# Kernel tuning notes

Hardware: AMD Instinct MI355X
Metric: run time of the kernel (lower is better)

## Reference

```python
import jax, jax.numpy as jnp
import numpy as np

N_EMBD = 384
N_HEAD = 6
HEAD_SIZE = N_EMBD // N_HEAD
D_FF = 4 * N_EMBD
LN_EPS = 1e-3  # keras LayerNormalization default epsilon


def setup_inputs() -> dict:
    key = jax.random.key(0)
    ks = jax.random.split(key, 12)
    B, T = 4, 2048
    s = 1.0 / np.sqrt(N_EMBD)
    return {
        "x": jax.random.normal(ks[0], (B, T, N_EMBD), dtype=jnp.float32),
        "Wq": jax.random.normal(ks[1], (N_EMBD, N_EMBD), dtype=jnp.float32) * s,
        "Wk": jax.random.normal(ks[2], (N_EMBD, N_EMBD), dtype=jnp.float32) * s,
        "Wv": jax.random.normal(ks[3], (N_EMBD, N_EMBD), dtype=jnp.float32) * s,
        "Wo": jax.random.normal(ks[4], (N_EMBD, N_EMBD), dtype=jnp.float32) * s,
        "bo": jnp.zeros((N_EMBD,), dtype=jnp.float32),
        "W1": jax.random.normal(ks[5], (N_EMBD, D_FF), dtype=jnp.float32) * s,
        "b1": jnp.zeros((D_FF,), dtype=jnp.float32),
        "W2": jax.random.normal(ks[6], (D_FF, N_EMBD), dtype=jnp.float32) * (1.0 / np.sqrt(D_FF)),
        "b2": jnp.zeros((N_EMBD,), dtype=jnp.float32),
        "g1": jnp.ones((N_EMBD,), dtype=jnp.float32),
        "be1": jnp.zeros((N_EMBD,), dtype=jnp.float32),
        "g2": jnp.ones((N_EMBD,), dtype=jnp.float32),
        "be2": jnp.zeros((N_EMBD,), dtype=jnp.float32),
    }


def _layer_norm(x, gamma, beta):
    mu = jnp.mean(x, axis=-1, keepdims=True)
    var = jnp.mean(jnp.square(x - mu), axis=-1, keepdims=True)
    return (x - mu) * jax.lax.rsqrt(var + LN_EPS) * gamma + beta


def _block(x, Wq, Wk, Wv, Wo, bo, W1, b1, W2, b2, g1, be1, g2, be2):
    B, T, C = x.shape
    H, D = N_HEAD, HEAD_SIZE
    q = (x @ Wq).reshape(B, T, H, D).transpose(0, 2, 1, 3)  # [B,H,T,D]
    k = (x @ Wk).reshape(B, T, H, D).transpose(0, 2, 1, 3)
    v = (x @ Wv).reshape(B, T, H, D).transpose(0, 2, 1, 3)
    scores = jnp.einsum("bhqd,bhkd->bhqk", q, k) / jnp.sqrt(jnp.float32(D))
    causal = jnp.tril(jnp.ones((T, T), dtype=bool))
    scores = jnp.where(causal, scores, jnp.float32(-1e9))
    attn = jax.nn.softmax(scores, axis=-1)  # dropout is identity at inference
    out = jnp.einsum("bhqk,bhkd->bhqd", attn, v)
    out = out.transpose(0, 2, 1, 3).reshape(B, T, H * D)
    y = out @ Wo + bo
    x = _layer_norm(x + y, g1, be1)
    y = jax.nn.relu(x @ W1 + b1) @ W2 + b2
    return _layer_norm(x + y, g2, be2)


def reference(x, Wq, Wk, Wv, Wo, bo, W1, b1, W2, b2, g1, be1, g2, be2):
    return _block(x, Wq, Wk, Wv, Wo, bo, W1, b1, W2, b2, g1, be1, g2, be2)
```

## Files before the change

### kernel.cpp

```cpp
#include <hip/hip_runtime.h>

#define C_DIM  384
#define HEADS  6
#define HD     64
#define FF_DIM 1536
#define LN_EPS 1e-3f
#define TSEQ   2048
#define BATCH  4
#define LOG2E  1.4426950408889634f
#define QK_SCALE 0.18033688011112042f

typedef __attribute__((ext_vector_type(2))) float          f32x2;
typedef __attribute__((ext_vector_type(4))) float          f32x4;
typedef __attribute__((ext_vector_type(4))) float          float4_t;
typedef __attribute__((ext_vector_type(8))) short          bfrag;
typedef __attribute__((ext_vector_type(4))) unsigned short ushort4_t;
typedef __attribute__((ext_vector_type(8))) unsigned short ushort8_t;

__device__ inline unsigned short f2bf(float f) {
    unsigned int u = __builtin_bit_cast(unsigned int, f);
    u += 0x7fff + ((u >> 16) & 1);
    return (unsigned short)(u >> 16);
}
__device__ inline unsigned short f2bf_t(float f) {
    return (unsigned short)(__builtin_bit_cast(unsigned int, f) >> 16);
}
__device__ inline float bf2f(unsigned short u) {
    return __builtin_bit_cast(float, (unsigned int)u << 16);
}

__device__ inline void gload_lds16(const void* g, void* l) {
    __builtin_amdgcn_global_load_lds(
        (const __attribute__((address_space(1))) unsigned int*)g,
        (__attribute__((address_space(3))) unsigned int*)l,
        16, 0, 0);
}

__device__ inline int xcd_chunk(int flat, int nwg) {
    return (flat >> 3) + (flat & 7) * (nwg >> 3);
}

__global__ __launch_bounds__(256)
void prep_all(const float* __restrict__ Wq, const float* __restrict__ Wk,
              const float* __restrict__ Wv, const float* __restrict__ Wo,
              const float* __restrict__ W1, const float* __restrict__ W2,
              const float* __restrict__ x,
              unsigned short* __restrict__ Dqkv, unsigned short* __restrict__ Do_,
              unsigned short* __restrict__ D1, unsigned short* __restrict__ D2,
              unsigned short* __restrict__ xb)
{
    __shared__ float tile[32][33];
    const int bidx = blockIdx.x;
    const int tx = threadIdx.x, ty = threadIdx.y;
    if (bidx >= 1728) {
        const int i = (bidx - 1728) * 256 + ty * 32 + tx;
        float4_t v = ((const float4_t*)x)[i];
        ushort4_t o = { f2bf(v.x), f2bf(v.y), f2bf(v.z), f2bf(v.w) };
        ((ushort4_t*)xb)[i] = o;
        return;
    }
    const float* W; unsigned short* D;
    int K, N, nx, ny;
    if (bidx < 576) {
        const int z = bidx / 144, r = bidx % 144;
        W = z == 0 ? Wq : (z == 1 ? Wk : (z == 2 ? Wv : Wo));
        D = z == 3 ? Do_ : Dqkv + (size_t)z * C_DIM * C_DIM;
        K = N = C_DIM; nx = r % 12; ny = r / 12;
    } else if (bidx < 1152) {
        const int r = bidx - 576;
        W = W1; D = D1; K = C_DIM; N = FF_DIM; nx = r % 48; ny = r / 48;
    } else {
        const int r = bidx - 1152;
        W = W2; D = D2; K = FF_DIM; N = C_DIM; nx = r % 12; ny = r / 12;
    }
    const int n0 = nx * 32, k0 = ny * 32;
    #pragma unroll
    for (int i = 0; i < 32; i += 8)
        tile[ty + i][tx] = W[(size_t)(k0 + ty + i) * N + n0 + tx];
    __syncthreads();
    #pragma unroll
    for (int i = 0; i < 32; i += 8)
        D[(size_t)(n0 + ty + i) * K + k0 + tx] = f2bf(tile[tx][ty + i]);
}

__global__ __launch_bounds__(256)
void vtrans_kernel(const unsigned short* __restrict__ qkv,
                   unsigned short* __restrict__ vt)
{
    __shared__ unsigned short tile[32][34];
    const int tx = threadIdx.x, ty = threadIdx.y;
    const int bh = blockIdx.z, b = bh / HEADS, h = bh % HEADS;
    const int t0 = blockIdx.x * 32, d0 = blockIdx.y * 32;
    #pragma unroll
    for (int i = 0; i < 32; i += 8)
        tile[ty + i][tx] = qkv[(size_t)(b * TSEQ + t0 + ty + i) * 1152 + 2 * C_DIM + h * HD + d0 + tx];
    __syncthreads();
    #pragma unroll
    for (int i = 0; i < 32; i += 8)
        vt[((size_t)bh * HD + d0 + ty + i) * TSEQ + t0 + tx] = tile[tx][ty + i];
}

template<int OBF16, int BIAS, int RELU, int QSCALE, int KSPLIT>
__global__ __launch_bounds__(256)
void gemm_lds(const unsigned short* __restrict__ A, const unsigned short* __restrict__ Bt,
              const float* __restrict__ bias, void* __restrict__ Cv,
              unsigned short* __restrict__ ktc,
              int M, int N, int K)
{
    __shared__ __align__(16) unsigned short As[16 * 512];
    __shared__ __align__(16) unsigned short Bs[16 * 512];

    const int t = threadIdx.x, lane = t & 63, w = t >> 6;
    const int ln16 = lane & 15, hi16 = lane >> 4;
    const int wr = w >> 1, wc = w & 1;
    const int nwg = gridDim.x * gridDim.y;
    const int L = xcd_chunk(blockIdx.y * gridDim.x + blockIdx.x, nwg);
    const int row0 = (L / gridDim.x) * 128, col0 = (L % gridDim.x) * 128;

    f32x4 acc[4][4] = {};

    for (int k0 = 0; k0 < K; k0 += 64) {
        #pragma unroll
        for (int i = 0; i < 4; ++i) {
            const int f  = w * 4 + i;
            const int ks = f >> 3, rf = f & 7;
            const int row = rf * 16 + ln16;
            const int kc  = k0 + ks * 32 + hi16 * 8;
            gload_lds16(&A [(size_t)(row0 + row) * K + kc], &As[f * 512]);
            gload_lds16(&Bt[(size_t)(col0 + row) * K + kc], &Bs[f * 512]);
        }
        __syncthreads();
        #pragma unroll
        for (int ks = 0; ks < 2; ++ks) {
            bfrag a[4], b[4];
            #pragma unroll
            for (int i = 0; i < 4; ++i)
                a[i] = *(const bfrag*)&As[(ks * 8 + wr * 4 + i) * 512 + lane * 8];
            #pragma unroll
            for (int j = 0; j < 4; ++j)
                b[j] = *(const bfrag*)&Bs[(ks * 8 + wc * 4 + j) * 512 + lane * 8];
            #pragma unroll
            for (int i = 0; i < 4; ++i)
                #pragma unroll
                for (int j = 0; j < 4; ++j)
                    acc[i][j] = __builtin_amdgcn_mfma_f32_16x16x32_bf16(a[i], b[j], acc[i][j], 0, 0, 0);
        }
        __syncthreads();
    }

    #pragma unroll
    for (int j = 0; j < 4; ++j) {
        const int cbase = col0 + wc * 64 + j * 16;
        const int col = cbase + ln16;
        const float bv = BIAS ? bias[col] : 0.0f;
        const float sc = (QSCALE && col < C_DIM) ? QK_SCALE : 1.0f;
        const bool kdest = KSPLIT && (cbase >= C_DIM) && (cbase < 2 * C_DIM);
        #pragma unroll
        for (int i = 0; i < 4; ++i) {
            #pragma unroll
            for (int e = 0; e < 4; ++e) {
                const int row = row0 + wr * 64 + i * 16 + hi16 * 4 + e;
                float v = acc[i][j][e] + bv;
                if (RELU) v = fmaxf(v, 0.0f);
                if (QSCALE) v *= sc;
                if (kdest) {
                    const int b  = row >> 11, tt = row & 2047;
                    const int hd = col - C_DIM;
                    const int bh = b * HEADS + (hd >> 6);
                    ktc[((size_t)bh * TSEQ + tt) * HD + (hd & 63)] = f2bf(v);
                } else if (OBF16) {
                    ((unsigned short*)Cv)[(size_t)row * N + col] = f2bf(v);
                } else {
                    ((float*)Cv)[(size_t)row * N + col] = v;
                }
            }
        }
    }
}

template<int OBF16, int BIAS, int RELU>
__global__ __launch_bounds__(256)
void gemm_lds64(const unsigned short* __restrict__ A, const unsigned short* __restrict__ Bt,
                const float* __restrict__ bias, void* __restrict__ Cv,
                int M, int N, int K)
{
    __shared__ __align__(16) unsigned short As[2][8 * 512];
    __shared__ __align__(16) unsigned short Bs[2][16 * 512];

    const int t = threadIdx.x, lane = t & 63, w = t >> 6;
    const int ln16 = lane & 15, hi16 = lane >> 4;
    const int wr = w >> 1, wc = w & 1;
    const int nwg = gridDim.x * gridDim.y;
    const int L = xcd_chunk(blockIdx.y * gridDim.x + blockIdx.x, nwg);
    const int row0 = (L / gridDim.x) * 64, col0 = (L % gridDim.x) * 128;

    f32x4 acc[2][4] = {};

    auto stage = [&](int bf, int k0) {
        #pragma unroll
        for (int i = 0; i < 2; ++i) {
            const int f  = w * 2 + i;
            const int ks = f >> 2, rf = f & 3;
            gload_lds16(&A[(size_t)(row0 + rf * 16 + ln16) * K + k0 + ks * 32 + hi16 * 8],
                        &As[bf][f * 512]);
        }
        #pragma unroll
        for (int i = 0; i < 4; ++i) {
            const int f  = w * 4 + i;
            const int ks = f >> 3, cf = f & 7;
            gload_lds16(&Bt[(size_t)(col0 + cf * 16 + ln16) * K + k0 + ks * 32 + hi16 * 8],
                        &Bs[bf][f * 512]);
        }
    };

    int buf = 0;
    stage(0, 0);
    __syncthreads();

    for (int k0 = 0; k0 < K; k0 += 64) {
        if (k0 + 64 < K) stage(buf ^ 1, k0 + 64);
        #pragma unroll
        for (int ks = 0; ks < 2; ++ks) {
            bfrag a[2], b[4];
            #pragma unroll
            for (int i = 0; i < 2; ++i)
                a[i] = *(const bfrag*)&As[buf][(ks * 4 + wr * 2 + i) * 512 + lane * 8];
            #pragma unroll
            for (int j = 0; j < 4; ++j)
                b[j] = *(const bfrag*)&Bs[buf][(ks * 8 + wc * 4 + j) * 512 + lane * 8];
            #pragma unroll
            for (int i = 0; i < 2; ++i)
                #pragma unroll
                for (int j = 0; j < 4; ++j)
                    acc[i][j] = __builtin_amdgcn_mfma_f32_16x16x32_bf16(a[i], b[j], acc[i][j], 0, 0, 0);
        }
        __syncthreads();
        buf ^= 1;
    }

    #pragma unroll
    for (int j = 0; j < 4; ++j) {
        const int col = col0 + wc * 64 + j * 16 + ln16;
        const float bv = BIAS ? bias[col] : 0.0f;
        #pragma unroll
        for (int i = 0; i < 2; ++i) {
            #pragma unroll
            for (int e = 0; e < 4; ++e) {
                const int row = row0 + wr * 32 + i * 16 + hi16 * 4 + e;
                float v = acc[i][j][e] + bv;
                if (RELU) v = fmaxf(v, 0.0f);
                if (OBF16) ((unsigned short*)Cv)[(size_t)row * N + col] = f2bf(v);
                else       ((float*)Cv)[(size_t)row * N + col] = v;
            }
        }
    }
}

__device__ inline void qk16(const bfrag (&qf)[2][2], const bfrag (&kf)[4][2],
                            f32x4 (&sf)[2][4])
{
    __builtin_amdgcn_s_setprio(1);
    #pragma unroll
    for (int jt = 0; jt < 4; ++jt)
        #pragma unroll
        for (int ks = 0; ks < 2; ++ks) {
            sf[0][jt] = __builtin_amdgcn_mfma_f32_16x16x32_bf16(qf[0][ks], kf[jt][ks], sf[0][jt], 0, 0, 0);
            sf[1][jt] = __builtin_amdgcn_mfma_f32_16x16x32_bf16(qf[1][ks], kf[jt][ks], sf[1][jt], 0, 0, 0);
        }
    __builtin_amdgcn_s_setprio(0);
}

__device__ inline void softmax_pv(f32x4 (&sf)[2][4], const bfrag (&vf)[4][2],
                                  f32x4 (&acc)[2][4],
                                  float (&mrow)[2][4], float (&lrow)[2][4],
                                  unsigned short (*Ps)[72],
                                  int tok0, int kt, bool last, int ln16, int hi16)
{
    float lmax[2][4];
    bool need = false;
    #pragma unroll
    for (int rf = 0; rf < 2; ++rf)
        #pragma unroll
        for (int e = 0; e < 4; ++e) {
            const int row = tok0 + rf * 16 + hi16 * 4 + e;
            float mx = -1e30f;
            #pragma unroll
            for (int jt = 0; jt < 4; ++jt) {
                float sv = sf[rf][jt][e];
                if (last && (kt * 64 + jt * 16 + ln16 > row)) sv = -1e30f;
                mx = fmaxf(mx, sv);
            }
            lmax[rf][e] = mx;
            need = need || (mx > mrow[rf][e] + 8.0f);
        }
    if (__any(need)) {
        #pragma unroll
        for (int rf = 0; rf < 2; ++rf)
            #pragma unroll
            for (int e = 0; e < 4; ++e) {
                float rm = lmax[rf][e];
                rm = fmaxf(rm, __shfl_xor(rm, 1));
                rm = fmaxf(rm, __shfl_xor(rm, 2));
                rm = fmaxf(rm, __shfl_xor(rm, 4));
                rm = fmaxf(rm, __shfl_xor(rm, 8));
                const float mn = fmaxf(mrow[rf][e], rm);
                const float corr = exp2f(mrow[rf][e] - mn);
                mrow[rf][e] = mn;
                lrow[rf][e] *= corr;
                #pragma unroll
                for (int dt = 0; dt < 4; ++dt) acc[rf][dt][e] *= corr;
            }
    }

    #pragma unroll
    for (int rf = 0; rf < 2; ++rf)
        #pragma unroll
        for (int jt = 0; jt < 4; ++jt)
            #pragma unroll
            for (int e = 0; e < 4; ++e) {
                const int row = tok0 + rf * 16 + hi16 * 4 + e;
                float sv = sf[rf][jt][e];
                if (last && (kt * 64 + jt * 16 + ln16 > row)) sv = -1e30f;
                const float pe = exp2f(sv - mrow[rf][e]);
                lrow[rf][e] += pe;
                Ps[rf * 16 + hi16 * 4 + e][jt * 16 + ln16] = f2bf_t(pe);
            }

    bfrag pf[2][2];
    #pragma unroll
    for (int rf = 0; rf < 2; ++rf)
        #pragma unroll
        for (int ks = 0; ks < 2; ++ks)
            pf[rf][ks] = *(const bfrag*)&Ps[rf * 16 + ln16][ks * 32 + hi16 * 8];
    __builtin_amdgcn_s_setprio(1);
    #pragma unroll
    for (int ks = 0; ks < 2; ++ks)
        #pragma unroll
        for (int rf = 0; rf < 2; ++rf)
            #pragma unroll
            for (int dt = 0; dt < 4; ++dt)
                acc[rf][dt] = __builtin_amdgcn_mfma_f32_16x16x32_bf16(pf[rf][ks], vf[dt][ks], acc[rf][dt], 0, 0, 0);
    __builtin_amdgcn_s_setprio(0);
}

__global__ __launch_bounds__(64)
void attn_kernel(const unsigned short* __restrict__ qkv,
                 const unsigned short* __restrict__ ktc,
                 const unsigned short* __restrict__ vt,
                 unsigned short* __restrict__ att,
                 unsigned short* __restrict__ pacc,
                 float* __restrict__ pml)
{
    __shared__ __align__(16) unsigned short Ps[32][72];
    const int lane = threadIdx.x;
    const int ln16 = lane & 15, hi16 = lane >> 4;
    const int bid = blockIdx.x;
    const int xcd = bid & 7;
    const int i   = bid >> 3;
    int bh, qw, kt0, kte, ck = 0;
    bool heavy;
    if (i < 192) {
        qw = 63 - (i / 6);
        const int r = i % 6;
        bh = xcd * 3 + (r >> 1);
        ck = r & 1;
        const int NT = (qw >> 1) + 1;
        const int half = NT >> 1;
        kt0 = ck ? half : 0;
        kte = ck ? NT : half;
        heavy = true;
    } else {
        const int j = i - 192;
        qw = 31 - (j / 3);
        bh = xcd * 3 + (j % 3);
        kt0 = 0;
        kte = (qw >> 1) + 1;
        heavy = false;
    }
    const int NTfull = (qw >> 1) + 1;
    const int b = bh / HEADS, h = bh % HEADS;
    const int tok0 = qw * 32;
    const size_t qrow0 = (size_t)b * TSEQ;

    bfrag qf[2][2];
    #pragma unroll
    for (int rf = 0; rf < 2; ++rf)
        #pragma unroll
        for (int ks = 0; ks < 2; ++ks)
            qf[rf][ks] = *(const bfrag*)&qkv[(qrow0 + tok0 + rf * 16 + ln16) * 1152 + h * HD + ks * 32 + hi16 * 8];

    f32x4 acc[2][4] = {};
    float mrow[2][4], lrow[2][4];
    #pragma unroll
    for (int rf = 0; rf < 2; ++rf)
        #pragma unroll
        for (int e = 0; e < 4; ++e) { mrow[rf][e] = -1e30f; lrow[rf][e] = 0.0f; }

    const unsigned short* Kb = ktc + (size_t)bh * TSEQ * HD;
    const unsigned short* Vb = vt  + (size_t)bh * HD * TSEQ;

    bfrag kf[4][2];
    #pragma unroll
    for (int jt = 0; jt < 4; ++jt)
        #pragma unroll
        for (int ks = 0; ks < 2; ++ks)
            kf[jt][ks] = *(const bfrag*)&Kb[(size_t)(kt0 * 64 + jt * 16 + ln16) * HD + ks * 32 + hi16 * 8];

    for (int kt = kt0; kt < kte; ++kt) {
        bfrag vf[4][2];
        #pragma unroll
        for (int dt = 0; dt < 4; ++dt)
            #pragma unroll
            for (int ks = 0; ks < 2; ++ks)
                vf[dt][ks] = *(const bfrag*)&Vb[(size_t)(dt * 16 + ln16) * TSEQ + kt * 64 + ks * 32 + hi16 * 8];

        f32x4 sf[2][4] = {};
        qk16(qf, kf, sf);

        if (kt + 1 < kte) {
            #pragma unroll
            for (int jt = 0; jt < 4; ++jt)
                #pragma unroll
                for (int ks = 0; ks < 2; ++ks)
                    kf[jt][ks] = *(const bfrag*)&Kb[(size_t)((kt + 1) * 64 + jt * 16 + ln16) * HD + ks * 32 + hi16 * 8];
        }

        softmax_pv(sf, vf, acc, mrow, lrow, Ps, tok0, kt, kt == NTfull - 1, ln16, hi16);
    }

    float lsum[2][4];
    #pragma unroll
    for (int rf = 0; rf < 2; ++rf)
        #pragma unroll
        for (int e = 0; e < 4; ++e) {
            float l = lrow[rf][e];
            l += __shfl_xor(l, 1);
            l += __shfl_xor(l, 2);
            l += __shfl_xor(l, 4);
            l += __shfl_xor(l, 8);
            lsum[rf][e] = l;
        }

    if (!heavy) {
        #pragma unroll
        for (int rf = 0; rf < 2; ++rf)
            #pragma unroll
            for (int e = 0; e < 4; ++e) {
                const float inv = 1.0f / lsum[rf][e];
                const size_t row = qrow0 + tok0 + rf * 16 + hi16 * 4 + e;
                #pragma unroll
                for (int dt = 0; dt < 4; ++dt)
                    att[row * C_DIM + h * HD + dt * 16 + ln16] = f2bf(acc[rf][dt][e] * inv);
            }
    } else {
        const int sidx = bh * 32 + (qw - 32);
        const size_t pb = (size_t)sidx * 2 + ck;
        #pragma unroll
        for (int rf = 0; rf < 2; ++rf)
            #pragma unroll
            for (int dt = 0; dt < 4; ++dt)
                #pragma unroll
                for (int e = 0; e < 4; ++e) {
                    const int row = rf * 16 + hi16 * 4 + e;
                    pacc[(pb * 32 + row) * 64 + dt * 16 + ln16] = f2bf(acc[rf][dt][e]);
                }
        if (ln16 == 0) {
            #pragma unroll
            for (int rf = 0; rf < 2; ++rf)
                #pragma unroll
                for (int e = 0; e < 4; ++e) {
                    const int row = rf * 16 + hi16 * 4 + e;
                    pml[pb * 64 + row * 2 + 0] = mrow[rf][e];
                    pml[pb * 64 + row * 2 + 1] = lsum[rf][e];
                }
        }
    }
}

__global__ __launch_bounds__(256)
void attn_combine(const unsigned short* __restrict__ pacc,
                  const float* __restrict__ pml,
                  unsigned short* __restrict__ att)
{
    const int sidx = blockIdx.x;
    const int bh = sidx >> 5;
    const int qw = 32 + (sidx & 31);
    const int b = bh / HEADS, h = bh % HEADS;
    const int tid = threadIdx.x;
    const int row = tid >> 3;
    const int d0  = (tid & 7) * 8;

    const float m0 = pml[((size_t)sidx * 2 + 0) * 64 + row * 2 + 0];
    const float l0 = pml[((size_t)sidx * 2 + 0) * 64 + row * 2 + 1];
    const float m1 = pml[((size_t)sidx * 2 + 1) * 64 + row * 2 + 0];
    const float l1 = pml[((size_t)sidx * 2 + 1) * 64 + row * 2 + 1];
    const float M  = fmaxf(m0, m1);
    const float w0 = exp2f(m0 - M), w1 = exp2f(m1 - M);
    const float invL = 1.0f / (l0 * w0 + l1 * w1);

    ushort8_t a0 = *(const ushort8_t*)&pacc[(((size_t)sidx * 2 + 0) * 32 + row) * 64 + d0];
    ushort8_t a1 = *(const ushort8_t*)&pacc[(((size_t)sidx * 2 + 1) * 32 + row) * 64 + d0];
    ushort8_t rv;
    #pragma unroll
    for (int k = 0; k < 8; ++k) {
        const float v0 = bf2f(a0[k]);
        const float v1 = bf2f(a1[k]);
        rv[k] = f2bf((v0 * w0 + v1 * w1) * invL);
    }
    const size_t grow = (size_t)b * TSEQ + qw * 32 + row;
    *(ushort8_t*)&att[grow * C_DIM + h * HD + d0] = rv;
}

template<int ABF16, int WF32, int WBF>
__global__ __launch_bounds__(256)
void ln_residual_kernel(const void* __restrict__ Av, const float* __restrict__ R,
                        const float* __restrict__ gamma, const float* __restrict__ beta,
                        float* __restrict__ out, unsigned short* __restrict__ outb, int Mrows)
{
    const int lane = threadIdx.x & 63;
    const int wv   = threadIdx.x >> 6;
    const int row  = blockIdx.x * 4 + wv;
    if (row >= Mrows) return;
    const size_t off = (size_t)row * C_DIM;

    float v[6];
    float sum = 0.0f;
    #pragma unroll
    for (int j = 0; j < 3; ++j) {
        const int c = lane * 2 + 128 * j;
        float a0, a1;
        if (ABF16) {
            const unsigned int u = *(const unsigned int*)&((const unsigned short*)Av)[off + c];
            a0 = bf2f((unsigned short)(u & 0xffff));
            a1 = bf2f((unsigned short)(u >> 16));
        } else {
            f32x2 a = *(const f32x2*)&((const float*)Av)[off + c];
            a0 = a.x; a1 = a.y;
        }
        f32x2 r = *(const f32x2*)&R[off + c];
        v[2 * j]     = a0 + r.x;
        v[2 * j + 1] = a1 + r.y;
        sum += v[2 * j] + v[2 * j + 1];
    }
    #pragma unroll
    for (int o = 1; o < 64; o <<= 1) sum += __shfl_xor(sum, o);
    const float mu = sum * (1.0f / C_DIM);

    float sq = 0.0f;
    #pragma unroll
    for (int j = 0; j < 6; ++j) { const float d = v[j] - mu; sq = fmaf(d, d, sq); }
    #pragma unroll
    for (int o = 1; o < 64; o <<= 1) sq += __shfl_xor(sq, o);
    const float rstd = rsqrtf(sq * (1.0f / C_DIM) + LN_EPS);

    #pragma unroll
    for (int j = 0; j < 3; ++j) {
        const int c = lane * 2 + 128 * j;
        f32x2 g  = *(const f32x2*)&gamma[c];
        f32x2 be = *(const f32x2*)&beta[c];
        const float r0 = (v[2 * j]     - mu) * rstd * g.x + be.x;
        const float r1 = (v[2 * j + 1] - mu) * rstd * g.y + be.y;
        if (WF32) { f32x2 o = { r0, r1 }; *(f32x2*)&out[off + c] = o; }
        if (WBF) {
            const unsigned int o = (unsigned int)f2bf(r0) | ((unsigned int)f2bf(r1) << 16);
            *(unsigned int*)&outb[off + c] = o;
        }
    }
}

extern "C" void kernel_launch(void* const* d_in, const int* in_sizes, int n_in,
                              void* d_out, int out_size, void* d_ws, size_t ws_size,
                              hipStream_t stream)
{
    const float* x   = (const float*)d_in[0];
    const float* Wq  = (const float*)d_in[1];
    const float* Wk  = (const float*)d_in[2];
    const float* Wv  = (const float*)d_in[3];
    const float* Wo  = (const float*)d_in[4];
    const float* bo  = (const float*)d_in[5];
    const float* W1  = (const float*)d_in[6];
    const float* b1  = (const float*)d_in[7];
    const float* W2  = (const float*)d_in[8];
    const float* b2  = (const float*)d_in[9];
    const float* g1  = (const float*)d_in[10];
    const float* be1 = (const float*)d_in[11];
    const float* g2  = (const float*)d_in[12];
    const float* be2 = (const float*)d_in[13];
    float* out = (float*)d_out;

    const int M = BATCH * TSEQ;
    const size_t MC = (size_t)M * C_DIM;

    char* ws = (char*)d_ws;
    unsigned short* qkv = (unsigned short*)ws;
    unsigned short* vt  = (unsigned short*)(ws + (size_t)M*1152*2);
    unsigned short* att = (unsigned short*)(ws + (size_t)M*1152*2 + (size_t)BATCH*HEADS*HD*TSEQ*2);
    unsigned short* h1  = (unsigned short*)ws;
    char* p2 = ws + (size_t)M*1152*2 + (size_t)BATCH*HEADS*HD*TSEQ*2 + MC*2;
    unsigned short* xb  = (unsigned short*)p2;
    float* y   = (float*)(p2 + MC*2);
    unsigned short* ktc = (unsigned short*)(p2 + MC*2 + MC*4);
    unsigned short* x1b = (unsigned short*)(p2 + MC*2 + 2*MC*4);
    char* p3 = p2 + MC*2 + 2*MC*4 + MC*2;
    unsigned short* Wqkv_t = (unsigned short*)p3;
    unsigned short* Wo_t   = Wqkv_t + (size_t)3*C_DIM*C_DIM;
    unsigned short* W1_t   = Wo_t   + (size_t)C_DIM*C_DIM;
    unsigned short* W2_t   = W1_t   + (size_t)FF_DIM*C_DIM;

    unsigned short* pacc = (unsigned short*)(p2 + MC*2);
    float* pml = (float*)(p2 + MC*2 + (size_t)1536*32*64*2);

    dim3 b256(256), b328(32, 8);

    prep_all<<<dim3(1728 + 3072), b328, 0, stream>>>(
        Wq, Wk, Wv, Wo, W1, W2, x, Wqkv_t, Wo_t, W1_t, W2_t, xb);

    gemm_lds<1, 0, 0, 1, 1><<<dim3(3*C_DIM/128, M/128), b256, 0, stream>>>(
        xb, Wqkv_t, nullptr, qkv, ktc, M, 3*C_DIM, C_DIM);

    vtrans_kernel<<<dim3(TSEQ/32, HD/32, BATCH*HEADS), b328, 0, stream>>>(qkv, vt);

    attn_kernel<<<dim3(2304), dim3(64), 0, stream>>>(qkv, ktc, vt, att, pacc, pml);
    attn_combine<<<dim3(768), b256, 0, stream>>>(pacc, pml, att);

    gemm_lds64<0, 1, 0><<<dim3(C_DIM/128, M/64), b256, 0, stream>>>(
        att, Wo_t, bo, y, M, C_DIM, C_DIM);

    ln_residual_kernel<0, 0, 1><<<dim3(M/4), b256, 0, stream>>>(
        x, y, g1, be1, nullptr, x1b, M);

    gemm_lds<1, 1, 1, 0, 0><<<dim3(FF_DIM/128, M/128), b256, 0, stream>>>(
        x1b, W1_t, b1, h1, nullptr, M, FF_DIM, C_DIM);

    gemm_lds64<0, 1, 0><<<dim3(C_DIM/128, M/64), b256, 0, stream>>>(
        h1, W2_t, b2, y, M, C_DIM, FF_DIM);

    ln_residual_kernel<1, 1, 0><<<dim3(M/4), b256, 0, stream>>>(
        x1b, y, g2, be2, out, nullptr, M);
}
```

Measured before the change: 191.9 us.

## Share K/V tiles across eight waves in LDS and drop split-K attention combine

Replaces the single-wave attention kernel with 512-thread blocks where eight waves each own a 32-row query slice of a 256-row tile, sharing double-buffered swizzled K/V tiles loaded to LDS via direct global-to-LDS loads. This removes redundant global K/V reads per wave and eliminates the split-KV partial write plus the separate combine kernel. The cost is only 192 blocks, fewer than the previous 2304, and causal imbalance inside a block: early-row waves sit idle at barriers while later waves finish their longer key ranges. The grid is also small relative to the CU count, so load balance across the device may suffer.

```diff
diff --git a/kernel.cpp b/kernel.cpp
--- a/kernel.cpp
+++ b/kernel.cpp
@@ -343,43 +343,29 @@
     __builtin_amdgcn_s_setprio(0);
 }
 
-__global__ __launch_bounds__(64)
-void attn_kernel(const unsigned short* __restrict__ qkv,
-                 const unsigned short* __restrict__ ktc,
-                 const unsigned short* __restrict__ vt,
-                 unsigned short* __restrict__ att,
-                 unsigned short* __restrict__ pacc,
-                 float* __restrict__ pml)
-{
-    __shared__ __align__(16) unsigned short Ps[32][72];
-    const int lane = threadIdx.x;
+__global__ __launch_bounds__(512)
+void attn8_kernel(const unsigned short* __restrict__ qkv,
+                  const unsigned short* __restrict__ ktc,
+                  const unsigned short* __restrict__ vt,
+                  unsigned short* __restrict__ att)
+{
+    __shared__ __align__(16) unsigned short Klds[2][4096];
+    __shared__ __align__(16) unsigned short Vlds[2][4096];
+    __shared__ __align__(16) unsigned short Ps[8][32][72];
+
+    const int tid  = threadIdx.x;
+    const int lane = tid & 63, wid = tid >> 6;
     const int ln16 = lane & 15, hi16 = lane >> 4;
     const int bid = blockIdx.x;
     const int xcd = bid & 7;
     const int i   = bid >> 3;
-    int bh, qw, kt0, kte, ck = 0;
-    bool heavy;
-    if (i < 192) {
-        qw = 63 - (i / 6);
-        const int r = i % 6;
-        bh = xcd * 3 + (r >> 1);
-        ck = r & 1;
-        const int NT = (qw >> 1) + 1;
-        const int half = NT >> 1;
-        kt0 = ck ? half : 0;
-        kte = ck ? NT : half;
-        heavy = true;
-    } else {
-        const int j = i - 192;
-        qw = 31 - (j / 3);
-        bh = xcd * 3 + (j % 3);
-        kt0 = 0;
-        kte = (qw >> 1) + 1;
-        heavy = false;
-    }
-    const int NTfull = (qw >> 1) + 1;
+    const int bh  = xcd * 3 + (i % 3);
+    const int qt  = 7 - (i / 3);
+    const int s   = qt * 8 + wid;
+    const int tok0 = s * 32;
+    const int NTw   = (s >> 1) + 1;
+    const int NTmax = qt * 4 + 4;
     const int b = bh / HEADS, h = bh % HEADS;
-    const int tok0 = qw * 32;
     const size_t qrow0 = (size_t)b * TSEQ;
 
     bfrag qf[2][2];
@@ -399,36 +385,50 @@
     const unsigned short* Kb = ktc + (size_t)bh * TSEQ * HD;
     const unsigned short* Vb = vt  + (size_t)bh * HD * TSEQ;
 
-    bfrag kf[4][2];
+    int off[4][2];
     #pragma unroll
     for (int jt = 0; jt < 4; ++jt)
         #pragma unroll
-        for (int ks = 0; ks < 2; ++ks)
-            kf[jt][ks] = *(const bfrag*)&Kb[(size_t)(kt0 * 64 + jt * 16 + ln16) * HD + ks * 32 + hi16 * 8];
-
-    for (int kt = kt0; kt < kte; ++kt) {
-        bfrag vf[4][2];
-        #pragma unroll
-        for (int dt = 0; dt < 4; ++dt)
-            #pragma unroll
-            for (int ks = 0; ks < 2; ++ks)
-                vf[dt][ks] = *(const bfrag*)&Vb[(size_t)(dt * 16 + ln16) * TSEQ + kt * 64 + ks * 32 + hi16 * 8];
-
-        f32x4 sf[2][4] = {};
-        qk16(qf, kf, sf);
-
-        if (kt + 1 < kte) {
+        for (int ks = 0; ks < 2; ++ks) {
+            const int row = jt * 16 + ln16;
+            off[jt][ks] = row * 128 + ((ks * 64 + hi16 * 16) ^ ((row & 7) << 4));
+        }
+
+    auto stage = [&](int bf, int kt) {
+        const int r   = tid >> 3;
+        const int s16 = (tid & 7) ^ (r & 7);
+        gload_lds16(&Kb[(size_t)(kt * 64 + r) * HD + s16 * 8], &Klds[bf][wid * 512]);
+        gload_lds16(&Vb[(size_t)r * TSEQ + kt * 64 + s16 * 8], &Vlds[bf][wid * 512]);
+    };
+
+    int buf = 0;
+    stage(0, 0);
+    __syncthreads();
+
+    for (int kt = 0; kt < NTmax; ++kt) {
+        if (kt + 1 < NTmax) stage(buf ^ 1, kt + 1);
+
+        if (kt < NTw) {
+            const char* Kb8 = (const char*)&Klds[buf][0];
+            const char* Vb8 = (const char*)&Vlds[buf][0];
+            bfrag kf[4][2], vf[4][2];
             #pragma unroll
             for (int jt = 0; jt < 4; ++jt)
                 #pragma unroll
-                for (int ks = 0; ks < 2; ++ks)
-                    kf[jt][ks] = *(const bfrag*)&Kb[(size_t)((kt + 1) * 64 + jt * 16 + ln16) * HD + ks * 32 + hi16 * 8];
-        }
-
-        softmax_pv(sf, vf, acc, mrow, lrow, Ps, tok0, kt, kt == NTfull - 1, ln16, hi16);
-    }
-
-    float lsum[2][4];
+                for (int ks = 0; ks < 2; ++ks) {
+                    kf[jt][ks] = *(const bfrag*)(Kb8 + off[jt][ks]);
+                    vf[jt][ks] = *(const bfrag*)(Vb8 + off[jt][ks]);
+                }
+
+            f32x4 sf[2][4] = {};
+            qk16(qf, kf, sf);
+            softmax_pv(sf, vf, acc, mrow, lrow, Ps[wid], tok0, kt, kt == NTw - 1, ln16, hi16);
+        }
+
+        __syncthreads();
+        buf ^= 1;
+    }
+
     #pragma unroll
     for (int rf = 0; rf < 2; ++rf)
         #pragma unroll
@@ -438,77 +438,12 @@
             l += __shfl_xor(l, 2);
             l += __shfl_xor(l, 4);
             l += __shfl_xor(l, 8);
-            lsum[rf][e] = l;
-        }
-
-    if (!heavy) {
-        #pragma unroll
-        for (int rf = 0; rf < 2; ++rf)
-            #pragma unroll
-            for (int e = 0; e < 4; ++e) {
-                const float inv = 1.0f / lsum[rf][e];
-                const size_t row = qrow0 + tok0 + rf * 16 + hi16 * 4 + e;
-                #pragma unroll
-                for (int dt = 0; dt < 4; ++dt)
-                    att[row * C_DIM + h * HD + dt * 16 + ln16] = f2bf(acc[rf][dt][e] * inv);
-            }
-    } else {
-        const int sidx = bh * 32 + (qw - 32);
-        const size_t pb = (size_t)sidx * 2 + ck;
-        #pragma unroll
-        for (int rf = 0; rf < 2; ++rf)
+            const float inv = 1.0f / l;
+            const size_t row = qrow0 + tok0 + rf * 16 + hi16 * 4 + e;
             #pragma unroll
             for (int dt = 0; dt < 4; ++dt)
-                #pragma unroll
-                for (int e = 0; e < 4; ++e) {
-                    const int row = rf * 16 + hi16 * 4 + e;
-                    pacc[(pb * 32 + row) * 64 + dt * 16 + ln16] = f2bf(acc[rf][dt][e]);
-                }
-        if (ln16 == 0) {
-            #pragma unroll
-            for (int rf = 0; rf < 2; ++rf)
-                #pragma unroll
-                for (int e = 0; e < 4; ++e) {
-                    const int row = rf * 16 + hi16 * 4 + e;
-                    pml[pb * 64 + row * 2 + 0] = mrow[rf][e];
-                    pml[pb * 64 + row * 2 + 1] = lsum[rf][e];
-                }
-        }
-    }
-}
-
-__global__ __launch_bounds__(256)
-void attn_combine(const unsigned short* __restrict__ pacc,
-                  const float* __restrict__ pml,
-                  unsigned short* __restrict__ att)
-{
-    const int sidx = blockIdx.x;
-    const int bh = sidx >> 5;
-    const int qw = 32 + (sidx & 31);
-    const int b = bh / HEADS, h = bh % HEADS;
-    const int tid = threadIdx.x;
-    const int row = tid >> 3;
-    const int d0  = (tid & 7) * 8;
-
-    const float m0 = pml[((size_t)sidx * 2 + 0) * 64 + row * 2 + 0];
-    const float l0 = pml[((size_t)sidx * 2 + 0) * 64 + row * 2 + 1];
-    const float m1 = pml[((size_t)sidx * 2 + 1) * 64 + row * 2 + 0];
-    const float l1 = pml[((size_t)sidx * 2 + 1) * 64 + row * 2 + 1];
-    const float M  = fmaxf(m0, m1);
-    const float w0 = exp2f(m0 - M), w1 = exp2f(m1 - M);
-    const float invL = 1.0f / (l0 * w0 + l1 * w1);
-
-    ushort8_t a0 = *(const ushort8_t*)&pacc[(((size_t)sidx * 2 + 0) * 32 + row) * 64 + d0];
-    ushort8_t a1 = *(const ushort8_t*)&pacc[(((size_t)sidx * 2 + 1) * 32 + row) * 64 + d0];
-    ushort8_t rv;
-    #pragma unroll
-    for (int k = 0; k < 8; ++k) {
-        const float v0 = bf2f(a0[k]);
-        const float v1 = bf2f(a1[k]);
-        rv[k] = f2bf((v0 * w0 + v1 * w1) * invL);
-    }
-    const size_t grow = (size_t)b * TSEQ + qw * 32 + row;
-    *(ushort8_t*)&att[grow * C_DIM + h * HD + d0] = rv;
+                att[row * C_DIM + h * HD + dt * 16 + ln16] = f2bf(acc[rf][dt][e] * inv);
+        }
 }
 
 template<int ABF16, int WF32, int WBF>
@@ -607,9 +542,6 @@
     unsigned short* W1_t   = Wo_t   + (size_t)C_DIM*C_DIM;
     unsigned short* W2_t   = W1_t   + (size_t)FF_DIM*C_DIM;
 
-    unsigned short* pacc = (unsigned short*)(p2 + MC*2);
-    float* pml = (float*)(p2 + MC*2 + (size_t)1536*32*64*2);
-
     dim3 b256(256), b328(32, 8);
 
     prep_all<<<dim3(1728 + 3072), b328, 0, stream>>>(
@@ -620,8 +552,7 @@
 
     vtrans_kernel<<<dim3(TSEQ/32, HD/32, BATCH*HEADS), b328, 0, stream>>>(qkv, vt);
 
-    attn_kernel<<<dim3(2304), dim3(64), 0, stream>>>(qkv, ktc, vt, att, pacc, pml);
-    attn_combine<<<dim3(768), b256, 0, stream>>>(pacc, pml, att);
+    attn8_kernel<<<dim3(192), dim3(512), 0, stream>>>(qkv, ktc, vt, att);
 
     gemm_lds64<0, 1, 0><<<dim3(C_DIM/128, M/64), b256, 0, stream>>>(
         att, Wo_t, bo, y, M, C_DIM, C_DIM);
```

New measurement: 213.7 us. 1.11x slower.
